# Performance work log

Hardware: AMD Instinct MI355X
Metric: run time of the kernel (lower is better)

## Reference

```python
import jax, jax.numpy as jnp
import numpy as np

N_HEAD = 16
D_MODEL = 1024
HEAD_DIM = D_MODEL // N_HEAD


def setup_inputs() -> dict:
    key = jax.random.key(0)
    ks = jax.random.split(key, 12)
    B, S, D = 2, 2048, D_MODEL
    scale = 1.0 / np.sqrt(D)
    inp = {
        "q": jax.random.normal(ks[0], (B, S, D), jnp.float32),
        "k": jax.random.normal(ks[1], (B, S, D), jnp.float32),
        "v": jax.random.normal(ks[2], (B, S, D), jnp.float32),
        "mask": jax.random.randint(ks[3], (B, 1, S, S), 0, 2, jnp.int32),
        "wq": jax.random.normal(ks[4], (D, D), jnp.float32) * scale,
        "bq": jnp.zeros((D,), jnp.float32),
        "wk": jax.random.normal(ks[5], (D, D), jnp.float32) * scale,
        "bk": jnp.zeros((D,), jnp.float32),
        "wv": jax.random.normal(ks[6], (D, D), jnp.float32) * scale,
        "bv": jnp.zeros((D,), jnp.float32),
        "wo": jax.random.normal(ks[7], (D, D), jnp.float32) * scale,
        "bo": jnp.zeros((D,), jnp.float32),
    }
    return inp


def _split_heads(x):
    B, S, D = x.shape
    return x.reshape(B, S, N_HEAD, HEAD_DIM).transpose(0, 2, 1, 3)  # [B,H,S,Hd]


def reference(q, k, v, mask, wq, bq, wk, bk, wv, bv, wo, bo):
    _q = _split_heads(q @ wq + bq)
    _k = _split_heads(k @ wk + bk)
    _v = _split_heads(v @ wv + bv)
    inv = 1.0 / (jnp.sqrt(jnp.float32(HEAD_DIM)) + 1e-8)
    score = jnp.einsum("bhqd,bhkd->bhqk", _q, _k) * inv
    score = score + mask.astype(score.dtype) * (-1e9)
    attn = jax.nn.softmax(score, axis=-1)
    ctx = jnp.einsum("bhqk,bhkd->bhqd", attn, _v)
    B, H, S, Hd = ctx.shape
    ctx = ctx.transpose(0, 2, 1, 3).reshape(B, S, H * Hd)
    return ctx @ wo + bo  # dropout is identity (eval / drop_rate=0)
```

## Files before the change

kernel.cpp:

```cpp
#include <hip/hip_runtime.h>

typedef unsigned short u16;
typedef __bf16 bf16x8_t __attribute__((ext_vector_type(8)));
typedef float  f32x4_t  __attribute__((ext_vector_type(4)));
typedef u16    us8_t    __attribute__((ext_vector_type(8)));
typedef u16    us4_t    __attribute__((ext_vector_type(4)));

__device__ __forceinline__ u16 f2bf(float f) {
    __bf16 h = (__bf16)f;
    return __builtin_bit_cast(u16, h);
}
__device__ __forceinline__ bf16x8_t ld_bf8(const u16* p) {
    us8_t u = *(const us8_t*)p;
    return __builtin_bit_cast(bf16x8_t, u);
}
__device__ __forceinline__ f32x4_t mfma16(bf16x8_t a, bf16x8_t b, f32x4_t c) {
    return __builtin_amdgcn_mfma_f32_16x16x32_bf16(a, b, c, 0, 0, 0);
}
__device__ __forceinline__ float exp2_fast(float x) {
#if __has_builtin(__builtin_amdgcn_exp2f)
    return __builtin_amdgcn_exp2f(x);
#else
    return exp2f(x);
#endif
}

__device__ __forceinline__ void dma16(const u16* g, u16* l) {
#if __has_builtin(__builtin_amdgcn_global_load_lds)
    __builtin_amdgcn_global_load_lds((const __attribute__((address_space(1))) unsigned int*)(g),
                                     (__attribute__((address_space(3))) unsigned int*)(l), 16, 0, 0);
#else
    *(us8_t*)l = *(const us8_t*)g;
#endif
}

__global__ __launch_bounds__(256) void prep_kernel(
    const float* __restrict__ q, const float* __restrict__ k, const float* __restrict__ v,
    const int* __restrict__ mask,
    const float* __restrict__ w0, const float* __restrict__ w1,
    const float* __restrict__ w2, const float* __restrict__ w3,
    u16* __restrict__ Qc, u16* __restrict__ Kc, u16* __restrict__ Vc,
    u16* __restrict__ Wt, unsigned* __restrict__ mp)
{
    __shared__ u16 t[64][65];
    const int bid = blockIdx.x, tid = threadIdx.x;
    if (bid < 6144) {
        const int z = bid >> 11, x = bid & 2047;
        const float* src = (z == 0) ? q : (z == 1) ? k : v;
        u16* dst = (z == 0) ? Qc : (z == 1) ? Kc : Vc;
        const size_t i = ((size_t)x * 256 + tid) * 8;
        float4 a = *(const float4*)(src + i);
        float4 b = *(const float4*)(src + i + 4);
        us8_t w;
        w[0] = f2bf(a.x); w[1] = f2bf(a.y); w[2] = f2bf(a.z); w[3] = f2bf(a.w);
        w[4] = f2bf(b.x); w[5] = f2bf(b.y); w[6] = f2bf(b.z); w[7] = f2bf(b.w);
        *(us8_t*)(dst + i) = w;
    } else if (bid < 7168) {
        const int r2 = bid - 6144;
        const int z = r2 >> 8, rem = r2 & 255;
        const float* src = (z == 0) ? w0 : (z == 1) ? w1 : (z == 2) ? w2 : w3;
        u16* dst = Wt + (size_t)z * 1048576;
        const int bk = (rem & 15) * 64, bn = (rem >> 4) * 64;
        const int r = tid >> 2, c4 = tid & 3;
        for (int i = 0; i < 4; i++) {
            float4 vv = *(const float4*)(src + (size_t)(bk + r) * 1024 + bn + c4 * 16 + i * 4);
            t[r][c4 * 16 + i * 4 + 0] = f2bf(vv.x);
            t[r][c4 * 16 + i * 4 + 1] = f2bf(vv.y);
            t[r][c4 * 16 + i * 4 + 2] = f2bf(vv.z);
            t[r][c4 * 16 + i * 4 + 3] = f2bf(vv.w);
        }
        __syncthreads();
        for (int i = 0; i < 2; i++) {
            us8_t w;
            for (int j = 0; j < 8; j++) w[j] = t[c4 * 16 + i * 8 + j][r];
            *(us8_t*)(dst + (size_t)(bn + r) * 1024 + bk + c4 * 16 + i * 8) = w;
        }
    } else {
        const int w = (bid - 7168) * 256 + tid;
        const int* src = mask + (size_t)w * 32;
        unsigned bits = 0u;
        for (int i = 0; i < 32; i += 4) {
            int4 vv = *(const int4*)(src + i);
            bits |= (unsigned)(vv.x != 0) << (i + 0);
            bits |= (unsigned)(vv.y != 0) << (i + 1);
            bits |= (unsigned)(vv.z != 0) << (i + 2);
            bits |= (unsigned)(vv.w != 0) << (i + 3);
        }
        mp[w] = bits;
    }
}

__global__ __launch_bounds__(256) void qkv_gemm_kernel(
    const u16* __restrict__ Qc, const u16* __restrict__ Kc, const u16* __restrict__ Vc,
    const u16* __restrict__ Wt,
    const float* __restrict__ bq, const float* __restrict__ bk, const float* __restrict__ bv,
    u16* __restrict__ Qh, u16* __restrict__ Kh, u16* __restrict__ Vtt)
{
    __shared__ __align__(16) u16 As[2][4096];
    __shared__ __align__(16) u16 Bs[2][4096];
    const int z = blockIdx.z;
    const u16* A = (z == 0) ? Qc : (z == 1) ? Kc : Vc;
    const u16* W = Wt + (size_t)z * 1048576;
    const float* bias = (z == 0) ? bq : (z == 1) ? bk : bv;

    const int m0 = blockIdx.x * 128, n0 = blockIdx.y * 128;
    const int tid = threadIdx.x, lane = tid & 63, wave = tid >> 6;
    const int l15 = lane & 15, quad = lane >> 4;
    const int wm = (wave & 1) * 64, wn = (wave >> 1) * 64;
    const int srow = lane >> 2, scol = (lane & 3) * 8;

    const f32x4_t z4 = {0.f, 0.f, 0.f, 0.f};
    f32x4_t acc[4][4];
    for (int i = 0; i < 4; i++) for (int j = 0; j < 4; j++) acc[i][j] = z4;

    auto stage = [&](int t, int bs) {
        const int k0 = t * 32;
        #pragma unroll
        for (int i = 0; i < 2; i++) {
            dma16(A + (size_t)(m0 + wave * 32 + i * 16 + srow) * 1024 + k0 + scol,
                  &As[bs][wave * 1024 + i * 512 + lane * 8]);
            dma16(W + (size_t)(n0 + wave * 32 + i * 16 + srow) * 1024 + k0 + scol,
                  &Bs[bs][wave * 1024 + i * 512 + lane * 8]);
        }
    };

    stage(0, 0);

    for (int t = 0; t < 32; ++t) {
        const int bs = t & 1;
        __syncthreads();
        if (t < 31) stage(t + 1, bs ^ 1);

        bf16x8_t af[4], bfr[4];
        #pragma unroll
        for (int i = 0; i < 4; i++) af[i] = ld_bf8(&As[bs][(wm + i * 16 + l15) * 32 + quad * 8]);
        #pragma unroll
        for (int j = 0; j < 4; j++) bfr[j] = ld_bf8(&Bs[bs][(wn + j * 16 + l15) * 32 + quad * 8]);
        #pragma unroll
        for (int i = 0; i < 4; i++)
            #pragma unroll
            for (int j = 0; j < 4; j++)
                acc[i][j] = mfma16(af[i], bfr[j], acc[i][j]);
    }

    #pragma unroll
    for (int i = 0; i < 4; i++) {
        const int m = m0 + wm + i * 16 + quad * 4;
        #pragma unroll
        for (int j = 0; j < 4; j++) {
            const int gn = n0 + wn + j * 16 + l15;
            const float bb = bias[gn];
            const int h = gn >> 6, dh = gn & 63;
            if (z < 2) {
                u16* Y = z ? Kh : Qh;
                const int jc = dh >> 3, e = dh & 7;
                #pragma unroll
                for (int r = 0; r < 4; r++) {
                    const int mm = m + r;
                    const int b = mm >> 11, s = mm & 2047;
                    Y[((size_t)(b * 16 + h) * 2048 + s) * 64 + ((jc ^ (s & 7)) * 8) + e] =
                        f2bf(acc[i][j][r] + bb);
                }
            } else {
                const int b = m >> 11, sh = m & 2047, kt2 = sh >> 7, sl = sh & 127;
                const int poslow = ((sl >> 4) & 1) * 4;
                const int chunk = (sl >> 5) * 4 + ((sl >> 2) & 3);
                us4_t w4;
                #pragma unroll
                for (int r = 0; r < 4; r++) w4[r] = f2bf(acc[i][j][r] + bb);
                size_t off = (((size_t)(b * 16 + h) * 16 + kt2) * 8192)
                           + (size_t)dh * 128 + ((chunk ^ (dh & 7)) * 8) + poslow;
                *(us4_t*)&Vtt[off] = w4;
            }
        }
    }
}

__global__ __launch_bounds__(256) void out_gemm_kernel(
    const u16* __restrict__ X, const u16* __restrict__ Wt,
    const float* __restrict__ bias, float* __restrict__ Y)
{
    __shared__ __align__(16) u16 As[2][2048];
    __shared__ __align__(16) u16 Bs[2][4096];
    const int m0 = blockIdx.x * 64, n0 = blockIdx.y * 128;
    const int tid = threadIdx.x, lane = tid & 63, wave = tid >> 6;
    const int l15 = lane & 15, quad = lane >> 4;
    const int wm = (wave & 1) * 32, wn = (wave >> 1) * 64;
    const int srow = lane >> 2, scol = (lane & 3) * 8;

    const f32x4_t z4 = {0.f, 0.f, 0.f, 0.f};
    f32x4_t acc[2][4];
    for (int i = 0; i < 2; i++) for (int j = 0; j < 4; j++) acc[i][j] = z4;

    auto stage = [&](int t, int bs) {
        const int k0 = t * 32;
        dma16(X + (size_t)(m0 + wave * 16 + srow) * 1024 + k0 + scol,
              &As[bs][wave * 512 + lane * 8]);
        #pragma unroll
        for (int i = 0; i < 2; i++)
            dma16(Wt + (size_t)(n0 + wave * 32 + i * 16 + srow) * 1024 + k0 + scol,
                  &Bs[bs][wave * 1024 + i * 512 + lane * 8]);
    };

    stage(0, 0);

    for (int t = 0; t < 32; ++t) {
        const int bs = t & 1;
        __syncthreads();
        if (t < 31) stage(t + 1, bs ^ 1);

        bf16x8_t af[2], bfr[4];
        #pragma unroll
        for (int i = 0; i < 2; i++) af[i] = ld_bf8(&As[bs][(wm + i * 16 + l15) * 32 + quad * 8]);
        #pragma unroll
        for (int j = 0; j < 4; j++) bfr[j] = ld_bf8(&Bs[bs][(wn + j * 16 + l15) * 32 + quad * 8]);
        #pragma unroll
        for (int i = 0; i < 2; i++)
            #pragma unroll
            for (int j = 0; j < 4; j++)
                acc[i][j] = mfma16(af[i], bfr[j], acc[i][j]);
    }

    #pragma unroll
    for (int i = 0; i < 2; i++) {
        const int m = m0 + wm + i * 16 + quad * 4;
        #pragma unroll
        for (int j = 0; j < 4; j++) {
            const int gn = n0 + wn + j * 16 + l15;
            const float bb = bias[gn];
            #pragma unroll
            for (int r = 0; r < 4; r++)
                Y[(size_t)(m + r) * 1024 + gn] = acc[i][j][r] + bb;
        }
    }
}

__global__ __launch_bounds__(256, 4) void attn_kernel(
    const u16* __restrict__ Qh, const u16* __restrict__ Kh,
    const u16* __restrict__ Vtt, const unsigned* __restrict__ mp,
    u16* __restrict__ C)
{
    __shared__ __align__(16) u16 Ks[2][4096];
    __shared__ __align__(16) u16 Vs[2][4096];
    const int h = blockIdx.x, qb = blockIdx.y, b = blockIdx.z;
    const int tid = threadIdx.x, lane = tid & 63, wave = tid >> 6;
    const int l15 = lane & 15, quad = lane >> 4;
    const int q0 = qb * 64 + wave * 16;
    const int grow = b * 2048 + q0;
    const size_t headoff = (size_t)(b * 16 + h) * 131072;
    const u16* Qg = Qh + headoff;
    const u16* Kg = Kh + headoff;
    const u16* Vg = Vtt + headoff;

    bf16x8_t aq[2];
    #pragma unroll
    for (int ks = 0; ks < 2; ks++)
        aq[ks] = ld_bf8(Qg + (size_t)(q0 + l15) * 64 + (((ks * 4 + quad) ^ (l15 & 7)) * 8));

    us8_t ones_u;
    #pragma unroll
    for (int i = 0; i < 8; i++) ones_u[i] = 0x3F80;
    const bf16x8_t ones = __builtin_bit_cast(bf16x8_t, ones_u);

    const f32x4_t z4 = {0.f, 0.f, 0.f, 0.f};
    f32x4_t o[4];
    #pragma unroll
    for (int i = 0; i < 4; i++) o[i] = z4;
    f32x4_t osum = z4;

    const int swA = (quad ^ (l15 & 7)) * 8;
    const int swB = ((4 + quad) ^ (l15 & 7)) * 8;

    const unsigned* mrow = mp + (size_t)(b * 2048 + q0 + l15) * 64;

    auto stage = [&](int kt, int bs) {
        const u16* kg = Kg + kt * 4096 + wave * 1024;
        const u16* vg = Vg + (kt >> 1) * 8192 + (kt & 1) * 64;
        u16* kl = &Ks[bs][wave * 1024];
        u16* vl = &Vs[bs][wave * 1024];
        #pragma unroll
        for (int i = 0; i < 2; i++) {
            dma16(kg + i * 512 + lane * 8, kl + i * 512 + lane * 8);
            dma16(vg + (size_t)(wave * 16 + i * 8 + (lane >> 3)) * 128 + (lane & 7) * 8,
                  vl + i * 512 + lane * 8);
        }
    };

    stage(0, 0);

    for (int kt = 0; kt < 32; ++kt) {
        const int bs = kt & 1;
        __syncthreads();
        if (kt < 31) stage(kt + 1, bs ^ 1);

        const int2 mv = *(const int2*)(mrow + kt * 2);

        f32x4_t sc[4];
        __builtin_amdgcn_s_setprio(1);
        #pragma unroll
        for (int st = 0; st < 4; st++) {
            const u16* kp = &Ks[bs][(st * 16 + l15) * 64];
            bf16x8_t k0 = ld_bf8(kp + swA);
            bf16x8_t k1 = ld_bf8(kp + swB);
            sc[st] = mfma16(k1, aq[1], mfma16(k0, aq[0], z4));
        }
        __builtin_amdgcn_s_setprio(0);

        us8_t ap[2];
        #pragma unroll
        for (int st = 0; st < 4; st++) {
            const unsigned w = (st < 2) ? (unsigned)mv.x : (unsigned)mv.y;
            const int shbase = ((st & 1) << 4) + quad * 4;
            #pragma unroll
            for (int r = 0; r < 4; r++) {
                const bool msk = (w >> (shbase + r)) & 1u;
                const float t = fmaf(sc[st][r], 0.18033688011f, msk ? -1e5f : -17.312340491f);
                ap[st >> 1][((st & 1) << 2) + r] = f2bf(exp2_fast(t));
            }
        }

        __builtin_amdgcn_s_setprio(1);
        #pragma unroll
        for (int c = 0; c < 2; c++) {
            bf16x8_t a = __builtin_bit_cast(bf16x8_t, ap[c]);
            osum = mfma16(a, ones, osum);
            #pragma unroll
            for (int nt = 0; nt < 4; nt++) {
                bf16x8_t bv = ld_bf8(&Vs[bs][(nt * 16 + l15) * 64
                                             + (((c * 4 + quad) ^ (l15 & 7)) * 8)]);
                o[nt] = mfma16(a, bv, o[nt]);
            }
        }
        __builtin_amdgcn_s_setprio(0);
    }

    #pragma unroll
    for (int r = 0; r < 4; r++) {
        const float invl = 1.0f / osum[r];
        const int row = grow + quad * 4 + r;
        #pragma unroll
        for (int nt = 0; nt < 4; nt++)
            C[(size_t)row * 1024 + h * 64 + nt * 16 + l15] = f2bf(o[nt][r] * invl);
    }
}

extern "C" void kernel_launch(void* const* d_in, const int* in_sizes, int n_in,
                              void* d_out, int out_size, void* d_ws, size_t ws_size,
                              hipStream_t stream) {
    const float* q    = (const float*)d_in[0];
    const float* k    = (const float*)d_in[1];
    const float* v    = (const float*)d_in[2];
    const int*   mask = (const int*)d_in[3];
    const float* wq   = (const float*)d_in[4];
    const float* bq   = (const float*)d_in[5];
    const float* wk   = (const float*)d_in[6];
    const float* bk   = (const float*)d_in[7];
    const float* wv   = (const float*)d_in[8];
    const float* bv   = (const float*)d_in[9];
    const float* wo   = (const float*)d_in[10];
    const float* bo   = (const float*)d_in[11];
    float* out = (float*)d_out;

    char* ws = (char*)d_ws;
    const size_t MB = 1ull << 20;
    u16* Wt      = (u16*)(ws);
    u16* Qc      = (u16*)(ws + 8 * MB);
    u16* Kc      = (u16*)(ws + 16 * MB);
    u16* Vc      = (u16*)(ws + 24 * MB);
    u16* Qhh     = (u16*)(ws + 32 * MB);
    u16* Khh     = (u16*)(ws + 40 * MB);
    u16* Vtt     = (u16*)(ws + 48 * MB);
    u16* CT      = (u16*)(ws + 8 * MB);
    unsigned* mp = (unsigned*)(ws + 56 * MB);

    prep_kernel<<<dim3(8192), 256, 0, stream>>>(
        q, k, v, mask, wq, wk, wv, wo, Qc, Kc, Vc, Wt, mp);

    qkv_gemm_kernel<<<dim3(32, 8, 3), 256, 0, stream>>>(
        Qc, Kc, Vc, Wt, bq, bk, bv, Qhh, Khh, Vtt);

    attn_kernel<<<dim3(16, 32, 2), 256, 0, stream>>>(Qhh, Khh, Vtt, mp, CT);

    out_gemm_kernel<<<dim3(64, 8), 256, 0, stream>>>(CT, Wt + 3ull * 1048576, bo, out);
}
```

Baseline: 261.1 us.

## Fuse fp32-to-bf16 activation conversion into QKV GEMM and use mask-bias LUT

Removes the separate pass that converted q/k/v from fp32 to bf16 in the prep kernel. The QKV GEMM now loads fp32 A tiles into registers, converts them, and writes them to LDS after the MFMA work, so the prep stage no longer writes and re-reads a bf16 copy. In exchange the GEMM's A operand now moves twice as many bytes per tile and uses plain register staging instead of direct-to-LDS DMA. The attention kernel also swaps per-element mask-bit selects for a 16-entry float4 LDS lookup indexed by a mask nibble.

```diff
diff --git a/kernel.cpp b/kernel.cpp
--- a/kernel.cpp
+++ b/kernel.cpp
@@ -35,29 +35,15 @@
 }
 
 __global__ __launch_bounds__(256) void prep_kernel(
-    const float* __restrict__ q, const float* __restrict__ k, const float* __restrict__ v,
     const int* __restrict__ mask,
     const float* __restrict__ w0, const float* __restrict__ w1,
     const float* __restrict__ w2, const float* __restrict__ w3,
-    u16* __restrict__ Qc, u16* __restrict__ Kc, u16* __restrict__ Vc,
     u16* __restrict__ Wt, unsigned* __restrict__ mp)
 {
     __shared__ u16 t[64][65];
     const int bid = blockIdx.x, tid = threadIdx.x;
-    if (bid < 6144) {
-        const int z = bid >> 11, x = bid & 2047;
-        const float* src = (z == 0) ? q : (z == 1) ? k : v;
-        u16* dst = (z == 0) ? Qc : (z == 1) ? Kc : Vc;
-        const size_t i = ((size_t)x * 256 + tid) * 8;
-        float4 a = *(const float4*)(src + i);
-        float4 b = *(const float4*)(src + i + 4);
-        us8_t w;
-        w[0] = f2bf(a.x); w[1] = f2bf(a.y); w[2] = f2bf(a.z); w[3] = f2bf(a.w);
-        w[4] = f2bf(b.x); w[5] = f2bf(b.y); w[6] = f2bf(b.z); w[7] = f2bf(b.w);
-        *(us8_t*)(dst + i) = w;
-    } else if (bid < 7168) {
-        const int r2 = bid - 6144;
-        const int z = r2 >> 8, rem = r2 & 255;
+    if (bid < 1024) {
+        const int z = bid >> 8, rem = bid & 255;
         const float* src = (z == 0) ? w0 : (z == 1) ? w1 : (z == 2) ? w2 : w3;
         u16* dst = Wt + (size_t)z * 1048576;
         const int bk = (rem & 15) * 64, bn = (rem >> 4) * 64;
@@ -76,7 +62,7 @@
             *(us8_t*)(dst + (size_t)(bn + r) * 1024 + bk + c4 * 16 + i * 8) = w;
         }
     } else {
-        const int w = (bid - 7168) * 256 + tid;
+        const int w = (bid - 1024) * 256 + tid;
         const int* src = mask + (size_t)w * 32;
         unsigned bits = 0u;
         for (int i = 0; i < 32; i += 4) {
@@ -91,7 +77,7 @@
 }
 
 __global__ __launch_bounds__(256) void qkv_gemm_kernel(
-    const u16* __restrict__ Qc, const u16* __restrict__ Kc, const u16* __restrict__ Vc,
+    const float* __restrict__ q, const float* __restrict__ k, const float* __restrict__ v,
     const u16* __restrict__ Wt,
     const float* __restrict__ bq, const float* __restrict__ bk, const float* __restrict__ bv,
     u16* __restrict__ Qh, u16* __restrict__ Kh, u16* __restrict__ Vtt)
@@ -99,7 +85,7 @@
     __shared__ __align__(16) u16 As[2][4096];
     __shared__ __align__(16) u16 Bs[2][4096];
     const int z = blockIdx.z;
-    const u16* A = (z == 0) ? Qc : (z == 1) ? Kc : Vc;
+    const float* A = (z == 0) ? q : (z == 1) ? k : v;
     const u16* W = Wt + (size_t)z * 1048576;
     const float* bias = (z == 0) ? bq : (z == 1) ? bk : bv;
 
@@ -113,23 +99,47 @@
     f32x4_t acc[4][4];
     for (int i = 0; i < 4; i++) for (int j = 0; j < 4; j++) acc[i][j] = z4;
 
-    auto stage = [&](int t, int bs) {
+    float4 ar[2][2];
+
+    auto loadA = [&](int t) {
         const int k0 = t * 32;
         #pragma unroll
         for (int i = 0; i < 2; i++) {
-            dma16(A + (size_t)(m0 + wave * 32 + i * 16 + srow) * 1024 + k0 + scol,
-                  &As[bs][wave * 1024 + i * 512 + lane * 8]);
+            const float* src = A + (size_t)(m0 + wave * 32 + i * 16 + srow) * 1024 + k0 + scol;
+            ar[i][0] = *(const float4*)src;
+            ar[i][1] = *(const float4*)(src + 4);
+        }
+    };
+    auto writeA = [&](int bs) {
+        #pragma unroll
+        for (int i = 0; i < 2; i++) {
+            us8_t w8;
+            w8[0] = f2bf(ar[i][0].x); w8[1] = f2bf(ar[i][0].y);
+            w8[2] = f2bf(ar[i][0].z); w8[3] = f2bf(ar[i][0].w);
+            w8[4] = f2bf(ar[i][1].x); w8[5] = f2bf(ar[i][1].y);
+            w8[6] = f2bf(ar[i][1].z); w8[7] = f2bf(ar[i][1].w);
+            *(us8_t*)&As[bs][wave * 1024 + i * 512 + lane * 8] = w8;
+        }
+    };
+    auto stageW = [&](int t, int bs) {
+        const int k0 = t * 32;
+        #pragma unroll
+        for (int i = 0; i < 2; i++)
             dma16(W + (size_t)(n0 + wave * 32 + i * 16 + srow) * 1024 + k0 + scol,
                   &Bs[bs][wave * 1024 + i * 512 + lane * 8]);
-        }
     };
 
-    stage(0, 0);
+    stageW(0, 0);
+    loadA(0);
+    writeA(0);
 
     for (int t = 0; t < 32; ++t) {
         const int bs = t & 1;
         __syncthreads();
-        if (t < 31) stage(t + 1, bs ^ 1);
+        if (t < 31) {
+            stageW(t + 1, bs ^ 1);
+            loadA(t + 1);
+        }
 
         bf16x8_t af[4], bfr[4];
         #pragma unroll
@@ -141,6 +151,8 @@
             #pragma unroll
             for (int j = 0; j < 4; j++)
                 acc[i][j] = mfma16(af[i], bfr[j], acc[i][j]);
+
+        if (t < 31) writeA(bs ^ 1);
     }
 
     #pragma unroll
@@ -242,6 +254,7 @@
 {
     __shared__ __align__(16) u16 Ks[2][4096];
     __shared__ __align__(16) u16 Vs[2][4096];
+    __shared__ __align__(16) float4 lut[16];
     const int h = blockIdx.x, qb = blockIdx.y, b = blockIdx.z;
     const int tid = threadIdx.x, lane = tid & 63, wave = tid >> 6;
     const int l15 = lane & 15, quad = lane >> 4;
@@ -252,6 +265,15 @@
     const u16* Kg = Kh + headoff;
     const u16* Vg = Vtt + headoff;
 
+    if (tid < 16) {
+        float4 bv4;
+        bv4.x = (tid & 1) ? -1e5f : -17.312340491f;
+        bv4.y = (tid & 2) ? -1e5f : -17.312340491f;
+        bv4.z = (tid & 4) ? -1e5f : -17.312340491f;
+        bv4.w = (tid & 8) ? -1e5f : -17.312340491f;
+        lut[tid] = bv4;
+    }
+
     bf16x8_t aq[2];
     #pragma unroll
     for (int ks = 0; ks < 2; ks++)
@@ -310,13 +332,12 @@
         #pragma unroll
         for (int st = 0; st < 4; st++) {
             const unsigned w = (st < 2) ? (unsigned)mv.x : (unsigned)mv.y;
-            const int shbase = ((st & 1) << 4) + quad * 4;
-            #pragma unroll
-            for (int r = 0; r < 4; r++) {
-                const bool msk = (w >> (shbase + r)) & 1u;
-                const float t = fmaf(sc[st][r], 0.18033688011f, msk ? -1e5f : -17.312340491f);
-                ap[st >> 1][((st & 1) << 2) + r] = f2bf(exp2_fast(t));
-            }
+            const int nib = (w >> (((st & 1) << 4) + quad * 4)) & 15;
+            const float4 b4 = lut[nib];
+            ap[st >> 1][((st & 1) << 2) + 0] = f2bf(exp2_fast(fmaf(sc[st][0], 0.18033688011f, b4.x)));
+            ap[st >> 1][((st & 1) << 2) + 1] = f2bf(exp2_fast(fmaf(sc[st][1], 0.18033688011f, b4.y)));
+            ap[st >> 1][((st & 1) << 2) + 2] = f2bf(exp2_fast(fmaf(sc[st][2], 0.18033688011f, b4.z)));
+            ap[st >> 1][((st & 1) << 2) + 3] = f2bf(exp2_fast(fmaf(sc[st][3], 0.18033688011f, b4.w)));
         }
 
         __builtin_amdgcn_s_setprio(1);
@@ -364,20 +385,17 @@
     char* ws = (char*)d_ws;
     const size_t MB = 1ull << 20;
     u16* Wt      = (u16*)(ws);
-    u16* Qc      = (u16*)(ws + 8 * MB);
-    u16* Kc      = (u16*)(ws + 16 * MB);
-    u16* Vc      = (u16*)(ws + 24 * MB);
-    u16* Qhh     = (u16*)(ws + 32 * MB);
-    u16* Khh     = (u16*)(ws + 40 * MB);
-    u16* Vtt     = (u16*)(ws + 48 * MB);
-    u16* CT      = (u16*)(ws + 8 * MB);
-    unsigned* mp = (unsigned*)(ws + 56 * MB);
-
-    prep_kernel<<<dim3(8192), 256, 0, stream>>>(
-        q, k, v, mask, wq, wk, wv, wo, Qc, Kc, Vc, Wt, mp);
+    u16* Qhh     = (u16*)(ws + 8 * MB);
+    u16* Khh     = (u16*)(ws + 16 * MB);
+    u16* Vtt     = (u16*)(ws + 24 * MB);
+    u16* CT      = (u16*)(ws + 32 * MB);
+    unsigned* mp = (unsigned*)(ws + 40 * MB);
+
+    prep_kernel<<<dim3(2048), 256, 0, stream>>>(
+        mask, wq, wk, wv, wo, Wt, mp);
 
     qkv_gemm_kernel<<<dim3(32, 8, 3), 256, 0, stream>>>(
-        Qc, Kc, Vc, Wt, bq, bk, bv, Qhh, Khh, Vtt);
+        q, k, v, Wt, bq, bk, bv, Qhh, Khh, Vtt);
 
     attn_kernel<<<dim3(16, 32, 2), 256, 0, stream>>>(Qhh, Khh, Vtt, mp, CT);
 
```

Measured after the change: 270.2 us. 1.03x slower.
